# Optimization experiments

Measured on AMD Instinct MI355X. Metric: run time of the kernel, lower is better.

Reference implementation:

```python
import jax, jax.numpy as jnp
import numpy as np


def _conv1x1(x, w, b=None):
    # x: [B,C,H,W], w: [O,C]
    y = jnp.einsum('bchw,oc->bohw', x, w)
    if b is not None:
        y = y + b[None, :, None, None]
    return y


def _conv3x3_dilated(x, w, b, dil):
    p = dil  # padding == dilation keeps spatial size for 3x3 kernels
    y = jax.lax.conv_general_dilated(
        x, w, window_strides=(1, 1), padding=((p, p), (p, p)),
        rhs_dilation=(dil, dil), dimension_numbers=('NCHW', 'OIHW', 'NCHW'))
    return y + b[None, :, None, None]


def _upsample2x_align_corners(x):
    # bilinear, align_corners=True, scale factor 2
    B, C, H, W = x.shape
    oh, ow = 2 * H, 2 * W
    ys = jnp.linspace(0.0, H - 1.0, oh)
    xs = jnp.linspace(0.0, W - 1.0, ow)
    y0 = jnp.floor(ys).astype(jnp.int32)
    x0 = jnp.floor(xs).astype(jnp.int32)
    y1 = jnp.minimum(y0 + 1, H - 1)
    x1 = jnp.minimum(x0 + 1, W - 1)
    wy = (ys - y0)[None, None, :, None]
    wx = (xs - x0)[None, None, None, :]
    gt = x[:, :, y0, :]
    gb = x[:, :, y1, :]
    top = gt[:, :, :, x0] * (1 - wx) + gt[:, :, :, x1] * wx
    bot = gb[:, :, :, x0] * (1 - wx) + gb[:, :, :, x1] * wx
    return top * (1 - wy) + bot * wy


def _gr(ftr, ck_w, ck_b, avg_w, max_w, gcn_w):
    # GR module: attention-diagonal graph conv with degree normalization
    B, C, H, W = ftr.shape
    HW = H * W
    # ChannelAttention_diag -> diagonal entries cw: [B, M]
    avg = ftr.mean(axis=(2, 3))
    mx = ftr.max(axis=(2, 3))
    cw = jax.nn.sigmoid(jax.nn.relu(avg @ avg_w.T) + jax.nn.relu(mx @ max_w.T))  # [B,M]
    k = jax.nn.relu(_conv1x1(ftr, ck_w, ck_b)).reshape(B, -1, HW)  # [B,M,HW]
    q = jnp.swapaxes(k, 1, 2)  # [B,HW,M]
    # A = sigmoid(q @ diag(cw) @ k); degree d = rowsum(A)^(-1/2)
    A = jax.nn.sigmoid(jnp.einsum('bim,bm,bmj->bij', q, cw, k))  # [B,HW,HW]
    d = A.sum(axis=2) ** -0.5  # [B,HW]
    P = d[:, :, None] * q  # D^{-1/2} @ q, [B,HW,M]
    X = jnp.swapaxes(ftr.reshape(B, C, HW), 1, 2)  # [B,HW,C]
    PtX = jnp.einsum('bjm,bjc->bmc', P, X)  # [B,M,C]
    LX = X - jnp.einsum('bim,bmc->bic', P, cw[:, :, None] * PtX)
    Y = X + LX @ gcn_w  # GCN (no bias)
    return jnp.swapaxes(Y, 1, 2).reshape(B, C, H, W)


def setup_inputs() -> dict:
    key = jax.random.key(0)
    ks = jax.random.split(key, 20)
    B, C = 64, 1024
    Cq = C // 4  # 256
    Mi = Cq // 2  # 128, ChannelAttention inter channels
    s = 0.02
    inp = {
        'x_cur': jax.random.normal(ks[0], (B, C, 16, 16), jnp.float32),
        'x_lat': jax.random.normal(ks[1], (B, C, 8, 8), jnp.float32),
        'conv_w': jax.random.normal(ks[2], (Cq, C), jnp.float32) * s,
        'conv_b': jax.random.normal(ks[3], (Cq,), jnp.float32) * s,
        'conv1_w': jax.random.normal(ks[4], (C, Cq), jnp.float32) * s,
        'conv1_b': jax.random.normal(ks[5], (C,), jnp.float32) * s,
        'conv3_w': jax.random.normal(ks[6], (C, 3 * Cq), jnp.float32) * s,
        'conv3_b': jax.random.normal(ks[7], (C,), jnp.float32) * s,
        'rate0_w': jax.random.normal(ks[8], (Cq, C, 3, 3), jnp.float32) * s,
        'rate0_b': jax.random.normal(ks[9], (Cq,), jnp.float32) * s,
        'rate1_w': jax.random.normal(ks[10], (Cq, C, 3, 3), jnp.float32) * s,
        'rate1_b': jax.random.normal(ks[11], (Cq,), jnp.float32) * s,
        'rate2_w': jax.random.normal(ks[12], (Cq, C, 3, 3), jnp.float32) * s,
        'rate2_b': jax.random.normal(ks[13], (Cq,), jnp.float32) * s,
        'gr_ck_w': jax.random.normal(ks[14], (Mi, Cq), jnp.float32) * s,
        'gr_ck_b': jax.random.normal(ks[15], (Mi,), jnp.float32) * s,
        'gr_avg_w': jax.random.normal(ks[16], (Mi, Cq), jnp.float32) * s,
        'gr_max_w': jax.random.normal(ks[17], (Mi, Cq), jnp.float32) * s,
        'gr_gcn_w': jax.random.normal(ks[18], (Cq, Cq), jnp.float32) * s,
        'pre': 1,
    }
    return inp


def reference(x_cur, x_lat, conv_w, conv_b, conv1_w, conv1_b, conv3_w, conv3_b,
              rate0_w, rate0_b, rate1_w, rate1_b, rate2_w, rate2_b,
              gr_ck_w, gr_ck_b, gr_avg_w, gr_max_w, gr_gcn_w, pre):
    # pre == 1 path of Graph_aspp.forward
    gr_args = (gr_ck_w, gr_ck_b, gr_avg_w, gr_max_w, gr_gcn_w)
    x_sum = x_cur * _upsample2x_align_corners(x_lat) + x_cur
    f1 = _conv3x3_dilated(x_sum, rate0_w, rate0_b, 1) + _conv1x1(x_sum, conv_w, conv_b)
    x1 = _gr(f1, *gr_args)
    feature = _conv1x1(f1, conv1_w, conv1_b) + x_sum
    f2 = _conv3x3_dilated(feature, rate1_w, rate1_b, 2) + _conv1x1(feature, conv_w, conv_b)
    x2 = _gr(f2, *gr_args)
    feature = _conv1x1(f2, conv1_w, conv1_b) + x_sum
    f3 = _conv3x3_dilated(feature, rate2_w, rate2_b, 4) + _conv1x1(feature, conv_w, conv_b)
    x3 = _gr(f3, *gr_args)
    cat = jnp.concatenate((x1, x2, x3), axis=1)
    return _conv1x1(cat, conv3_w, conv3_b)
```

## Files before the change

kernel.cpp:

```cpp
#include <hip/hip_runtime.h>

typedef unsigned short ushort_t;
typedef unsigned int uint32;
typedef __attribute__((ext_vector_type(8))) unsigned short ushort8;
typedef __attribute__((ext_vector_type(8))) __bf16 bf16x8;
typedef __attribute__((ext_vector_type(4))) float f32x4;

__device__ __forceinline__ ushort_t f2b(float f) {
    union { float f; uint32 u; } v; v.f = f;
    uint32 r = v.u + 0x7fffu + ((v.u >> 16) & 1u);
    return (ushort_t)(r >> 16);
}
__device__ __forceinline__ float b2f(ushort_t b) {
    union { uint32 u; float f; } v; v.u = ((uint32)b) << 16;
    return v.f;
}
__device__ __forceinline__ float sigm(float x) { return 1.f / (1.f + __expf(-x)); }

__device__ __forceinline__ void gload_lds16(const void* g, void* l) {
    __builtin_amdgcn_global_load_lds(
        (__attribute__((address_space(1))) void*)g,
        (__attribute__((address_space(3))) void*)l, 16, 0, 0);
}

constexpr int EPI_RELU  = 1;
constexpr int EPI_FQ    = 2;
constexpr int EPI_SIG   = 3;
constexpr int EPI_XG    = 4;
constexpr int EPI_NEGCW = 5;
constexpr int EPI_Y     = 6;
constexpr int EPI_OUTT  = 7;

struct GemmP {
    const ushort_t* A; const ushort_t* B;
    const ushort_t* A2; const ushort_t* B2;
    long long aBatch, bBatch, a2Batch, b2Batch;
    int lda, ldb, lda2, ldb2;
    int Ksub, kSplit, dil;
    const float* bias;
    const ushort_t* res; long long resBatch; int ldres;
    ushort_t* obf; long long oBatch; int ldo;
    ushort_t* obf2;
    float* of32;
    const float* cw;
    const float* rscale;
    float* dsum;
    const ushort_t* zpage;
};

__global__ __launch_bounds__(256) void gemm_big(GemmP p) {
    __shared__ __align__(16) ushort_t aT[128 * 64];
    __shared__ __align__(16) ushort_t bT[128 * 64];
    const int tid = threadIdx.x;
    const int z = blockIdx.z;
    const int m0 = blockIdx.x * 128, n0 = blockIdx.y * 128;
    const int lane = tid & 63, wid = tid >> 6;
    const int l15 = lane & 15, l16 = lane >> 4;
    const int wr = wid >> 1, wc = wid & 1;
    const int lrow = lane >> 3;
    const int sgran = (lane & 7) ^ lrow;

    int ayy[4], axx[4];
    const ushort_t* aBase[4];
    const ushort_t* bBase[4];
#pragma unroll
    for (int i = 0; i < 4; ++i) {
        int row = wid * 32 + i * 8 + lrow;
        int m = m0 + row;
        int bb = m >> 8;
        ayy[i] = (m >> 4) & 15; axx[i] = m & 15;
        aBase[i] = p.A + (long long)bb * 262144 + sgran * 8;
        bBase[i] = p.B + (long long)(n0 + row) * p.ldb + sgran * 8;
    }

    f32x4 acc[4][4];
#pragma unroll
    for (int i = 0; i < 4; ++i)
#pragma unroll
        for (int j = 0; j < 4; ++j) acc[i][j] = (f32x4){0.f, 0.f, 0.f, 0.f};

    const int gk0 = z * p.kSplit;
    const int ntap = p.Ksub >> 10;
    for (int ti = 0; ti < ntap; ++ti) {
        const int tap = (gk0 >> 10) + ti;
        int dy = 0, dx = 0;
        if (tap < 9) { int ky = tap / 3; dy = (ky - 1) * p.dil; dx = (tap - ky * 3 - 1) * p.dil; }
        const ushort_t* gaA[4];
        const ushort_t* gaB[4];
#pragma unroll
        for (int i = 0; i < 4; ++i) {
            int iy = ayy[i] + dy, ix = axx[i] + dx;
            bool ok = ((unsigned)iy < 16u) && ((unsigned)ix < 16u);
            gaA[i] = ok ? (aBase[i] + (((iy << 4) + ix) << 10)) : (p.zpage + sgran * 8);
            gaB[i] = bBase[i] + (tap << 10);
        }
        for (int kk = 0; kk < 16; ++kk) {
            const int kin = kk << 6;
#pragma unroll
            for (int i = 0; i < 4; ++i)
                gload_lds16(gaA[i] + kin, &aT[(wid * 32 + i * 8) * 64]);
#pragma unroll
            for (int i = 0; i < 4; ++i)
                gload_lds16(gaB[i] + kin, &bT[(wid * 32 + i * 8) * 64]);
            asm volatile("s_waitcnt vmcnt(0)" ::: "memory");
            __syncthreads();
#pragma unroll
            for (int ks = 0; ks < 2; ++ks) {
                bf16x8 af[4], bfr[4];
#pragma unroll
                for (int mi = 0; mi < 4; ++mi) {
                    int rr = wr * 64 + mi * 16 + l15;
                    int cc = (ks * 32 + l16 * 8) ^ ((rr & 7) << 3);
                    af[mi] = __builtin_bit_cast(bf16x8, *(const ushort8*)&aT[rr * 64 + cc]);
                }
#pragma unroll
                for (int ni = 0; ni < 4; ++ni) {
                    int rr = wc * 64 + ni * 16 + l15;
                    int cc = (ks * 32 + l16 * 8) ^ ((rr & 7) << 3);
                    bfr[ni] = __builtin_bit_cast(bf16x8, *(const ushort8*)&bT[rr * 64 + cc]);
                }
#pragma unroll
                for (int mi = 0; mi < 4; ++mi)
#pragma unroll
                    for (int ni = 0; ni < 4; ++ni)
                        acc[mi][ni] = __builtin_amdgcn_mfma_f32_16x16x32_bf16(af[mi], bfr[ni], acc[mi][ni], 0, 0, 0);
            }
            __syncthreads();
        }
    }
#pragma unroll
    for (int mi = 0; mi < 4; ++mi)
#pragma unroll
        for (int ni = 0; ni < 4; ++ni) {
            int gcol = n0 + wc * 64 + ni * 16 + l15;
            int growb = m0 + wr * 64 + mi * 16 + l16 * 4;
#pragma unroll
            for (int r = 0; r < 4; ++r)
                p.obf[(long long)z * p.oBatch + (long long)(growb + r) * 256 + gcol] =
                    f2b(acc[mi][ni][r]);
        }
}

template<int BM, int BN, int AMODE, int EPI>
__device__ __forceinline__ void gemm_body(ushort_t* aT, ushort_t* bT,
                                          const GemmP& p, int z) {
    constexpr int APASS = BM / 32, BPASS = BN / 32;
    constexpr int MFRAG = BM / 32, NFRAG = BN / 32;
    const int tid = threadIdx.x;
    const int m0 = blockIdx.x * BM, n0 = blockIdx.y * BN;
    const int lane = tid & 63, wid = tid >> 6;
    const int l15 = lane & 15, l16 = lane >> 4;
    const int wr = wid >> 1, wc = wid & 1;
    const int srow = tid >> 3, scol = (tid & 7) * 8;
    const int swcol = scol ^ ((srow & 7) << 3);

    const ushort_t* aptr[APASS];
    const ushort_t* bptr[BPASS];
    const ushort_t* aptr2[APASS];
    const ushort_t* bptr2[BPASS];
    float rsA[APASS];
#pragma unroll
    for (int pi = 0; pi < APASS; ++pi)
        aptr[pi] = p.A + (long long)z * p.aBatch +
                   (long long)(m0 + pi * 32 + srow) * p.lda + scol;
#pragma unroll
    for (int pi = 0; pi < BPASS; ++pi)
        bptr[pi] = p.B + (long long)z * p.bBatch +
                   (long long)(n0 + pi * 32 + srow) * p.ldb + scol;
    if constexpr (AMODE == 2) {
#pragma unroll
        for (int pi = 0; pi < APASS; ++pi) {
            aptr2[pi] = p.A2 + (long long)z * p.a2Batch +
                        (long long)(m0 + pi * 32 + srow) * p.lda2 + scol;
            rsA[pi] = p.rscale[z * 256 + m0 + pi * 32 + srow];
        }
#pragma unroll
        for (int pi = 0; pi < BPASS; ++pi)
            bptr2[pi] = p.B2 + (long long)z * p.b2Batch +
                        (long long)(n0 + pi * 32 + srow) * p.ldb2 + scol;
    }

    f32x4 acc[MFRAG][NFRAG];
#pragma unroll
    for (int i = 0; i < MFRAG; ++i)
#pragma unroll
        for (int j = 0; j < NFRAG; ++j) acc[i][j] = (f32x4){0.f, 0.f, 0.f, 0.f};

    ushort8 ar[APASS], br[BPASS];
    auto ldg = [&](int gk) {
        if (AMODE == 2 && gk >= 256) {
            int g2 = gk - 256;
#pragma unroll
            for (int pi = 0; pi < APASS; ++pi) {
                ushort8 t8 = *(const ushort8*)(aptr2[pi] + g2);
#pragma unroll
                for (int k = 0; k < 8; ++k) t8[k] = f2b(b2f(t8[k]) * rsA[pi]);
                ar[pi] = t8;
            }
#pragma unroll
            for (int pi = 0; pi < BPASS; ++pi) br[pi] = *(const ushort8*)(bptr2[pi] + g2);
        } else if constexpr (AMODE == 3) {
#pragma unroll
            for (int pi = 0; pi < APASS; ++pi) {
                ushort8 t8 = *(const ushort8*)(aptr[pi] + gk);
#pragma unroll
                for (int k = 0; k < 8; ++k)
                    t8[k] = f2b(b2f(t8[k]) * p.cw[(z << 7) + gk + scol + k]);
                ar[pi] = t8;
            }
#pragma unroll
            for (int pi = 0; pi < BPASS; ++pi) br[pi] = *(const ushort8*)(bptr[pi] + gk);
        } else {
#pragma unroll
            for (int pi = 0; pi < APASS; ++pi) ar[pi] = *(const ushort8*)(aptr[pi] + gk);
#pragma unroll
            for (int pi = 0; pi < BPASS; ++pi) br[pi] = *(const ushort8*)(bptr[pi] + gk);
        }
    };

    const int gk0 = z * p.kSplit;
    ldg(gk0);
    const int iters = p.Ksub >> 6;
    for (int it = 0; it < iters; ++it) {
#pragma unroll
        for (int pi = 0; pi < APASS; ++pi)
            *(ushort8*)&aT[(pi * 32 + srow) * 64 + swcol] = ar[pi];
#pragma unroll
        for (int pi = 0; pi < BPASS; ++pi)
            *(ushort8*)&bT[(pi * 32 + srow) * 64 + swcol] = br[pi];
        __syncthreads();
        if (it + 1 < iters) ldg(gk0 + (it + 1) * 64);
#pragma unroll
        for (int ks = 0; ks < 2; ++ks) {
            bf16x8 af[MFRAG], bfr[NFRAG];
#pragma unroll
            for (int mi = 0; mi < MFRAG; ++mi) {
                int rr = wr * (BM / 2) + mi * 16 + l15;
                int cc = (ks * 32 + l16 * 8) ^ ((rr & 7) << 3);
                af[mi] = __builtin_bit_cast(bf16x8, *(const ushort8*)&aT[rr * 64 + cc]);
            }
#pragma unroll
            for (int ni = 0; ni < NFRAG; ++ni) {
                int rr = wc * (BN / 2) + ni * 16 + l15;
                int cc = (ks * 32 + l16 * 8) ^ ((rr & 7) << 3);
                bfr[ni] = __builtin_bit_cast(bf16x8, *(const ushort8*)&bT[rr * 64 + cc]);
            }
#pragma unroll
            for (int mi = 0; mi < MFRAG; ++mi)
#pragma unroll
                for (int ni = 0; ni < NFRAG; ++ni)
                    acc[mi][ni] = __builtin_amdgcn_mfma_f32_16x16x32_bf16(af[mi], bfr[ni], acc[mi][ni], 0, 0, 0);
        }
        __syncthreads();
    }

#pragma unroll
    for (int mi = 0; mi < MFRAG; ++mi) {
        if constexpr (EPI == EPI_SIG) {
#pragma unroll
            for (int r = 0; r < 4; ++r) {
                float sv = 0.f;
#pragma unroll
                for (int ni = 0; ni < NFRAG; ++ni) sv += sigm(acc[mi][ni][r]);
                sv += __shfl_xor(sv, 1); sv += __shfl_xor(sv, 2);
                sv += __shfl_xor(sv, 4); sv += __shfl_xor(sv, 8);
                if (l15 == 0) {
                    int grow = m0 + wr * (BM / 2) + mi * 16 + l16 * 4 + r;
                    int q8 = blockIdx.y * 2 + wc;
                    p.dsum[q8 * 16384 + z * 256 + grow] = sv;
                }
            }
        } else {
#pragma unroll
            for (int ni = 0; ni < NFRAG; ++ni) {
                int gcol = n0 + wc * (BN / 2) + ni * 16 + l15;
                int growb = m0 + wr * (BM / 2) + mi * 16 + l16 * 4;
#pragma unroll
                for (int r = 0; r < 4; ++r) {
                    int grow = growb + r;
                    float v = acc[mi][ni][r];
                    if constexpr (EPI == EPI_RELU) {
                        v += p.bias[gcol]; v = fmaxf(v, 0.f);
                        p.obf[(long long)grow * p.ldo + gcol] = f2b(v);
                    } else if constexpr (EPI == EPI_FQ) {
                        v += p.bias[gcol];
                        if (gcol < 1024) {
                            v += b2f(p.res[(long long)grow * 1024 + gcol]);
                            p.obf[(long long)grow * 1024 + gcol] = f2b(v);
                        } else {
                            v = fmaxf(v, 0.f);
                            p.obf2[(long long)grow * 128 + (gcol - 1024)] = f2b(v);
                        }
                    } else if constexpr (EPI == EPI_XG) {
                        p.obf[(long long)z * p.oBatch + (long long)grow * p.ldo + gcol] = f2b(v);
                    } else if constexpr (EPI == EPI_NEGCW) {
                        v *= -p.cw[z * 128 + gcol];
                        p.obf[(long long)z * p.oBatch + (long long)grow * p.ldo + gcol] = f2b(v);
                    } else if constexpr (EPI == EPI_Y) {
                        v = b2f(p.res[(long long)z * p.resBatch + (long long)grow * p.ldres + gcol]) + v;
                        p.obf[(long long)z * p.oBatch + (long long)grow * p.ldo + gcol] = f2b(v);
                    } else if constexpr (EPI == EPI_OUTT) {
                        v += p.bias[grow];
                        int bb = gcol >> 8, px = gcol & 255;
                        p.of32[((long long)bb * 1024 + grow) * 256 + px] = v;
                    }
                }
            }
        }
    }
}

template<int BM, int BN, int AMODE, int EPI>
__global__ __launch_bounds__(256) void gemm_k(GemmP p) {
    __shared__ __align__(16) ushort_t aT[BM * 64];
    __shared__ __align__(16) ushort_t bT[BN * 64];
    gemm_body<BM, BN, AMODE, EPI>(aT, bT, p, blockIdx.z);
}

__device__ __forceinline__ void pool_body(void* lds, const ushort_t* f,
                                          const float* aw, const float* mw,
                                          float* cw) {
    float* sa = (float*)lds;
    float* sm = sa + 256;
    int b = blockIdx.x, t = threadIdx.x;
    float s = 0.f, m = -3.4e38f;
    const ushort_t* base = f + (long long)b * 65536 + t;
    for (int px = 0; px < 256; ++px) { float v = b2f(base[px * 256]); s += v; m = fmaxf(m, v); }
    sa[t] = s * (1.f / 256.f);
    sm[t] = m;
    __syncthreads();
    if (t < 128) {
        float s1 = 0.f, s2 = 0.f;
        const float* a = aw + t * 256; const float* w = mw + t * 256;
        for (int c = 0; c < 256; ++c) { s1 += sa[c] * a[c]; s2 += sm[c] * w[c]; }
        s1 = fmaxf(s1, 0.f); s2 = fmaxf(s2, 0.f);
        cw[b * 128 + t] = sigm(s1 + s2);
    }
}

__global__ __launch_bounds__(256) void gemm_fqpool(GemmP p, const float* aw,
                                                   const float* mw, float* cw) {
    __shared__ __align__(16) ushort_t aT[128 * 64];
    __shared__ __align__(16) ushort_t bT[128 * 64];
    if (blockIdx.y == 9) {
        if (blockIdx.x < 64) pool_body(aT, p.A, aw, mw, cw);
        return;
    }
    gemm_body<128, 128, 0, EPI_FQ>(aT, bT, p, 0);
}

__global__ __launch_bounds__(256) void gemm_qpool(GemmP p, const float* aw,
                                                  const float* mw, float* cw) {
    __shared__ __align__(16) ushort_t aT[64 * 64];
    __shared__ __align__(16) ushort_t bT[64 * 64];
    if (blockIdx.y == 2) {
        if (blockIdx.x < 64) pool_body(aT, p.A, aw, mw, cw);
        return;
    }
    gemm_body<64, 64, 0, EPI_RELU>(aT, bT, p, 0);
}

__global__ __launch_bounds__(256) void gemm_sigxg(GemmP ps, GemmP px) {
    __shared__ __align__(16) ushort_t aT[64 * 64];
    __shared__ __align__(16) ushort_t bT[64 * 64];
    int z = blockIdx.z;
    if (z < 64) gemm_body<64, 64, 3, EPI_SIG>(aT, bT, ps, z);
    else        gemm_body<64, 64, 0, EPI_XG>(aT, bT, px, z - 64);
}


__global__ void k_combine(const ushort_t* __restrict__ t, const float* __restrict__ fbias_s,
                          ushort_t* __restrict__ f) {
    int idx = blockIdx.x * 256 + threadIdx.x;
    const long long N = 16384ll * 256;
    ushort8 a0 = *(const ushort8*)(t + (long long)idx * 8);
    ushort8 a1 = *(const ushort8*)(t + N + (long long)idx * 8);
    ushort8 a2 = *(const ushort8*)(t + 2 * N + (long long)idx * 8);
    ushort8 a3 = *(const ushort8*)(t + 3 * N + (long long)idx * 8);
    ushort8 a4 = *(const ushort8*)(t + 4 * N + (long long)idx * 8);
    int cb = (idx * 8) & 255;
    ushort8 o;
#pragma unroll
    for (int k = 0; k < 8; ++k)
        o[k] = f2b(b2f(a0[k]) + b2f(a1[k]) + b2f(a2[k]) + b2f(a3[k]) + b2f(a4[k]) + fbias_s[cb + k]);
    *(ushort8*)&f[(long long)idx * 8] = o;
}

__global__ void k_upsum(const float* __restrict__ xc, const float* __restrict__ xl,
                        ushort_t* __restrict__ xs) {
    __shared__ float lat[64 * 64];
    __shared__ ushort_t tile[64 * 258];
    int b = blockIdx.x, c0 = blockIdx.y * 64;
    int t = threadIdx.x;
    for (int i = t; i < 4096; i += 256)
        lat[i] = xl[((long long)(b * 1024 + c0 + (i >> 6))) * 64 + (i & 63)];
    __syncthreads();
    int y = t >> 4, x = t & 15;
    float fy = y * (7.f / 15.f); int y0 = (int)fy; float wy = fy - y0; int y1 = y0 + 1 > 7 ? 7 : y0 + 1;
    float fx = x * (7.f / 15.f); int x0 = (int)fx; float wx = fx - x0; int x1 = x0 + 1 > 7 ? 7 : x0 + 1;
    for (int cc = 0; cc < 64; ++cc) {
        float cur = xc[((long long)(b * 1024 + c0 + cc)) * 256 + t];
        const float* L = &lat[cc * 64];
        float tv = L[y0 * 8 + x0] * (1.f - wx) + L[y0 * 8 + x1] * wx;
        float bv = L[y1 * 8 + x0] * (1.f - wx) + L[y1 * 8 + x1] * wx;
        float up = tv + (bv - tv) * wy;
        tile[cc * 258 + t] = f2b(cur * (1.f + up));
    }
    __syncthreads();
    for (int i = t; i < 16384; i += 256) {
        int px = i >> 6, cc = i & 63;
        xs[((long long)(b * 256 + px)) * 1024 + c0 + cc] = tile[cc * 258 + px];
    }
}

__global__ void k_pscale(const ushort_t* __restrict__ q, const float* __restrict__ dsum8,
                         float* __restrict__ dscale, ushort_t* __restrict__ Pt) {
    __shared__ ushort_t t[128][130];
    __shared__ float dd[128];
    int jh = blockIdx.x, b = blockIdx.y;
    int j0 = jh * 128;
    int tid = threadIdx.x;
    if (tid < 128) {
        int pix = b * 256 + j0 + tid;
        float s = 0.f;
#pragma unroll
        for (int qs = 0; qs < 8; ++qs) s += dsum8[qs * 16384 + pix];
        float r = rsqrtf(s);
        dd[tid] = r;
        dscale[pix] = r;
    }
    __syncthreads();
    int jr = tid >> 7, m = tid & 127;
    for (int i = 0; i < 64; ++i) {
        int j = i * 2 + jr;
        long long qi = ((long long)(b * 256 + j0 + j)) * 128 + m;
        t[j][m] = f2b(dd[j] * b2f(q[qi]));
    }
    __syncthreads();
    for (int i = 0; i < 64; ++i) {
        int mm = i * 2 + jr;
        Pt[((long long)b << 15) + (mm << 8) + j0 + m] = t[m][mm];
    }
}

__global__ void k_packall(const float* r0, const float* r1, const float* r2,
                          const float* convw, const float* c1w, const float* c3w,
                          const float* ckw, const float* gcnw,
                          const float* rb0, const float* rb1, const float* rb2,
                          const float* cb, const float* c1b, const float* ckbias,
                          ushort_t* wbig3, ushort_t* wfq, ushort_t* w3b,
                          ushort_t* gcnT, float* fqbias, float* fbias,
                          ushort_t* zpage) {
    int blk = blockIdx.x, tid = threadIdx.x;
    if (blk < 768) {
        __shared__ float lw[10240];
        int s = blk >> 8, o = blk & 255;
        const float* rate = s == 0 ? r0 : (s == 1 ? r1 : r2);
        for (int i = tid; i < 9216; i += 256) lw[i] = rate[(long long)o * 9216 + i];
        for (int i = tid; i < 1024; i += 256) lw[9216 + i] = convw[(long long)o * 1024 + i];
        __syncthreads();
        ushort_t* dst = wbig3 + (long long)blk * 10240;
        for (int i = tid; i < 10240; i += 256) {
            int tap = i >> 10, ci = i & 1023;
            float v = (tap < 9) ? lw[ci * 9 + tap] : lw[9216 + ci];
            dst[i] = f2b(v);
        }
        return;
    }
    const int R1 = 262144;
    const int R2 = R1 + 32768;
    const int R3 = R2 + 786432;
    const int R4 = R3 + 65536;
    const int R5 = R4 + 1152;
    const int R6 = R5 + 768;
    const int R7 = R6 + 4096;
    int base = (blk - 768) * 2048 + tid * 8;
#pragma unroll
    for (int k = 0; k < 8; ++k) {
        int i = base + k;
        if (i >= R7) return;
        if (i < R1) wfq[i] = f2b(c1w[i]);
        else if (i < R2) wfq[i] = f2b(ckw[i - R1]);
        else if (i < R3) w3b[i - R2] = f2b(c3w[i - R2]);
        else if (i < R4) {
            int ii = i - R3; int c2 = ii >> 8, c1 = ii & 255;
            gcnT[ii] = f2b(gcnw[c1 * 256 + c2]);
        } else if (i < R5) {
            int ii = i - R4;
            fqbias[ii] = (ii < 1024) ? c1b[ii] : ckbias[ii - 1024];
        } else if (i < R6) {
            int ii = i - R5; int s = ii >> 8, t = ii & 255;
            const float* rb = s == 0 ? rb0 : (s == 1 ? rb1 : rb2);
            fbias[ii] = rb[t] + cb[t];
        } else {
            zpage[i - R6] = 0;
        }
    }
}

__global__ void k_sentinel(float* o, int n, float v) {
    int i = blockIdx.x * 256 + threadIdx.x; if (i < n) o[i] = v;
}

extern "C" void kernel_launch(void* const* d_in, const int* in_sizes, int n_in,
                              void* d_out, int out_size, void* d_ws, size_t ws_size,
                              hipStream_t stream) {
    const float* x_cur  = (const float*)d_in[0];
    const float* x_lat  = (const float*)d_in[1];
    const float* conv_w = (const float*)d_in[2];
    const float* conv_b = (const float*)d_in[3];
    const float* conv1_w = (const float*)d_in[4];
    const float* conv1_b = (const float*)d_in[5];
    const float* conv3_w = (const float*)d_in[6];
    const float* conv3_b = (const float*)d_in[7];
    const float* rate_w[3] = {(const float*)d_in[8], (const float*)d_in[10], (const float*)d_in[12]};
    const float* rate_b[3] = {(const float*)d_in[9], (const float*)d_in[11], (const float*)d_in[13]};
    const float* ck_w  = (const float*)d_in[14];
    const float* ck_b  = (const float*)d_in[15];
    const float* avg_w = (const float*)d_in[16];
    const float* max_w = (const float*)d_in[17];
    const float* gcn_w = (const float*)d_in[18];
    float* out = (float*)d_out;

    char* w = (char*)d_ws;
    auto take = [&](size_t bytes) { void* p = (void*)w; w += (bytes + 255) & ~(size_t)255; return p; };
    ushort_t* xsum   = (ushort_t*)take(16384ll * 1024 * 2);
    ushort_t* feat   = (ushort_t*)take(16384ll * 1024 * 2);
    ushort_t* fbuf   = (ushort_t*)take(16384ll * 256 * 2);
    ushort_t* xgt    = (ushort_t*)take(64ll * 256 * 256 * 2);
    ushort_t* qbuf   = (ushort_t*)take(16384ll * 128 * 2);
    ushort_t* Pt     = (ushort_t*)take(64ll * 128 * 256 * 2);
    ushort_t* Htn    = (ushort_t*)take(64ll * 256 * 128 * 2);
    ushort_t* wbig3  = (ushort_t*)take(3ll * 256 * 10240 * 2);
    ushort_t* wfq    = (ushort_t*)take(1152ll * 256 * 2);
    ushort_t* w3b    = (ushort_t*)take(1024ll * 768 * 2);
    ushort_t* gcnT   = (ushort_t*)take(256ll * 256 * 2);
    ushort_t* zpage  = (ushort_t*)take(8192);
    float*    fqbias = (float*)take(1152 * 4);
    float*    fbias  = (float*)take(3 * 256 * 4);
    float*    cwb    = (float*)take(64 * 128 * 4);
    float*    dscale = (float*)take(64 * 256 * 4);
    float*    dsum8  = (float*)take(8ll * 64 * 256 * 4);
    ushort_t* catb   = (ushort_t*)take(16384ll * 768 * 2);
    ushort_t* ftmp   = (ushort_t*)take(5ll * 16384 * 256 * 2);
    size_t need = (size_t)(w - (char*)d_ws);

    if (need > ws_size) {
        float v = 1.0e6f + (float)(ws_size >> 20);
        k_sentinel<<<(out_size + 255) / 256, 256, 0, stream>>>(out, out_size, v);
        return;
    }

    k_packall<<<768 + 563, 256, 0, stream>>>(
        rate_w[0], rate_w[1], rate_w[2], conv_w, conv1_w, conv3_w, ck_w, gcn_w,
        rate_b[0], rate_b[1], rate_b[2], conv_b, conv1_b, ck_b,
        wbig3, wfq, w3b, gcnT, fqbias, fbias, zpage);
    k_upsum<<<dim3(64, 16), 256, 0, stream>>>(x_cur, x_lat, xsum);

    for (int s = 0; s < 3; ++s) {
        {
            GemmP p{};
            p.A = (s == 0) ? xsum : feat;
            p.B = wbig3 + (long long)s * 256 * 10240; p.ldb = 10240;
            p.Ksub = 2048; p.kSplit = 2048; p.dil = 1 << s;
            p.obf = ftmp; p.oBatch = 16384ll * 256;
            p.zpage = zpage;
            gemm_big<<<dim3(128, 2, 5), 256, 0, stream>>>(p);
        }
        k_combine<<<2048, 256, 0, stream>>>(ftmp, fbias + s * 256, fbuf);
        if (s < 2) {
            GemmP p{};
            p.A = fbuf; p.lda = 256; p.B = wfq; p.ldb = 256;
            p.Ksub = 256; p.bias = fqbias;
            p.res = xsum;
            p.obf = feat; p.obf2 = qbuf;
            gemm_fqpool<<<dim3(128, 10, 1), 256, 0, stream>>>(p, avg_w, max_w, cwb);
        } else {
            GemmP p{};
            p.A = fbuf; p.lda = 256; p.B = wfq + 1024 * 256; p.ldb = 256;
            p.Ksub = 256;
            p.bias = ck_b; p.obf = qbuf; p.ldo = 128;
            gemm_qpool<<<dim3(256, 3, 1), 256, 0, stream>>>(p, avg_w, max_w, cwb);
        }
        {
            GemmP ps{};
            ps.A = qbuf; ps.aBatch = 32768; ps.lda = 128;
            ps.B = qbuf; ps.bBatch = 32768; ps.ldb = 128;
            ps.Ksub = 128; ps.dsum = dsum8; ps.cw = cwb;
            GemmP px{};
            px.A = gcnT; px.aBatch = 0;     px.lda = 256;
            px.B = fbuf; px.bBatch = 65536; px.ldb = 256;
            px.Ksub = 256;
            px.obf = xgt; px.oBatch = 65536; px.ldo = 256;
            gemm_sigxg<<<dim3(4, 4, 128), 256, 0, stream>>>(ps, px);
        }
        k_pscale<<<dim3(2, 64), 256, 0, stream>>>(qbuf, dsum8, dscale, Pt);
        {
            GemmP p{};
            p.A = xgt; p.aBatch = 65536; p.lda = 256;
            p.B = Pt;  p.bBatch = 32768; p.ldb = 256;
            p.Ksub = 256; p.cw = cwb;
            p.obf = Htn; p.oBatch = 32768; p.ldo = 128;
            gemm_k<64, 64, 0, EPI_NEGCW><<<dim3(4, 2, 64), 256, 0, stream>>>(p);
        }
        {
            GemmP p{};
            p.A = fbuf; p.aBatch = 65536; p.lda = 256;
            p.B = gcnT; p.bBatch = 0;     p.ldb = 256;
            p.A2 = qbuf; p.a2Batch = 32768; p.lda2 = 128; p.rscale = dscale;
            p.B2 = Htn;  p.b2Batch = 32768; p.ldb2 = 128;
            p.Ksub = 384;
            p.res = fbuf; p.resBatch = 65536; p.ldres = 256;
            p.obf = catb + s * 256; p.oBatch = 256ll * 768; p.ldo = 768;
            gemm_k<64, 64, 2, EPI_Y><<<dim3(4, 4, 64), 256, 0, stream>>>(p);
        }
    }
    {
        GemmP p{};
        p.A = w3b;  p.lda = 768;
        p.B = catb; p.ldb = 768;
        p.Ksub = 768; p.bias = conv3_b; p.of32 = out;
        gemm_k<64, 128, 0, EPI_OUTT><<<dim3(16, 128, 1), 256, 0, stream>>>(p);
    }
}
```

Before: 646.4 us.

## Software-pipeline GR stages across ASPP stages by fusing independent GEMMs into shared launches

Restructures the three-stage loop so each stage's GR work (sigmoid-degree GEMM, X·G GEMM, Htn and Y GEMMs) runs in the same kernel launch as the next stage's big dilated conv GEMM or FQ GEMM. Block indices are dispatched to different GEMM bodies through flattened grid coordinates. fbuf, qbuf and cw are double-buffered so adjacent stages do not conflict. The aim is fewer launches and better CU fill for the small under-occupying GR GEMMs, at the cost of more complex dispatch and a larger shared-memory footprint for the small tiles.

```diff
diff --git a/kernel.cpp b/kernel.cpp
--- a/kernel.cpp
+++ b/kernel.cpp
@@ -48,12 +48,10 @@
     const ushort_t* zpage;
 };
 
-__global__ __launch_bounds__(256) void gemm_big(GemmP p) {
-    __shared__ __align__(16) ushort_t aT[128 * 64];
-    __shared__ __align__(16) ushort_t bT[128 * 64];
+__device__ __forceinline__ void big_body(ushort_t* aT, ushort_t* bT,
+                                         const GemmP& p, int bx, int by, int z) {
     const int tid = threadIdx.x;
-    const int z = blockIdx.z;
-    const int m0 = blockIdx.x * 128, n0 = blockIdx.y * 128;
+    const int m0 = bx * 128, n0 = by * 128;
     const int lane = tid & 63, wid = tid >> 6;
     const int l15 = lane & 15, l16 = lane >> 4;
     const int wr = wid >> 1, wc = wid & 1;
@@ -143,11 +141,11 @@
 
 template<int BM, int BN, int AMODE, int EPI>
 __device__ __forceinline__ void gemm_body(ushort_t* aT, ushort_t* bT,
-                                          const GemmP& p, int z) {
+                                          const GemmP& p, int bx, int by, int z) {
     constexpr int APASS = BM / 32, BPASS = BN / 32;
     constexpr int MFRAG = BM / 32, NFRAG = BN / 32;
     const int tid = threadIdx.x;
-    const int m0 = blockIdx.x * BM, n0 = blockIdx.y * BN;
+    const int m0 = bx * BM, n0 = by * BN;
     const int lane = tid & 63, wid = tid >> 6;
     const int l15 = lane & 15, l16 = lane >> 4;
     const int wr = wid >> 1, wc = wid & 1;
@@ -266,7 +264,7 @@
                 sv += __shfl_xor(sv, 4); sv += __shfl_xor(sv, 8);
                 if (l15 == 0) {
                     int grow = m0 + wr * (BM / 2) + mi * 16 + l16 * 4 + r;
-                    int q8 = blockIdx.y * 2 + wc;
+                    int q8 = by * 2 + wc;
                     p.dsum[q8 * 16384 + z * 256 + grow] = sv;
                 }
             }
@@ -314,15 +312,15 @@
 __global__ __launch_bounds__(256) void gemm_k(GemmP p) {
     __shared__ __align__(16) ushort_t aT[BM * 64];
     __shared__ __align__(16) ushort_t bT[BN * 64];
-    gemm_body<BM, BN, AMODE, EPI>(aT, bT, p, blockIdx.z);
-}
-
-__device__ __forceinline__ void pool_body(void* lds, const ushort_t* f,
+    gemm_body<BM, BN, AMODE, EPI>(aT, bT, p, blockIdx.x, blockIdx.y, blockIdx.z);
+}
+
+__device__ __forceinline__ void pool_body(void* lds, int b, const ushort_t* f,
                                           const float* aw, const float* mw,
                                           float* cw) {
     float* sa = (float*)lds;
     float* sm = sa + 256;
-    int b = blockIdx.x, t = threadIdx.x;
+    int t = threadIdx.x;
     float s = 0.f, m = -3.4e38f;
     const ushort_t* base = f + (long long)b * 65536 + t;
     for (int px = 0; px < 256; ++px) { float v = b2f(base[px * 256]); s += v; m = fmaxf(m, v); }
@@ -338,34 +336,51 @@
     }
 }
 
-__global__ __launch_bounds__(256) void gemm_fqpool(GemmP p, const float* aw,
-                                                   const float* mw, float* cw) {
-    __shared__ __align__(16) ushort_t aT[128 * 64];
-    __shared__ __align__(16) ushort_t bT[128 * 64];
-    if (blockIdx.y == 9) {
-        if (blockIdx.x < 64) pool_body(aT, p.A, aw, mw, cw);
+__global__ __launch_bounds__(256) void k_big_sig_y(GemmP pb, GemmP ps, GemmP px,
+                                                   GemmP py) {
+    __shared__ __align__(16) ushort_t lds[2 * 128 * 64];
+    int z = blockIdx.z;
+    if (z < 5) { big_body(lds, lds + 8192, pb, blockIdx.x, blockIdx.y, z); return; }
+    if (z < 13) {
+        int flat = (z - 5) * 256 + blockIdx.y * 128 + blockIdx.x;
+        int bx = flat & 3, by = (flat >> 2) & 3, bz = flat >> 4;
+        if (bz < 64) gemm_body<64, 64, 3, EPI_SIG>(lds, lds + 4096, ps, bx, by, bz);
+        else         gemm_body<64, 64, 0, EPI_XG>(lds, lds + 4096, px, bx, by, bz - 64);
         return;
     }
-    gemm_body<128, 128, 0, EPI_FQ>(aT, bT, p, 0);
-}
-
-__global__ __launch_bounds__(256) void gemm_qpool(GemmP p, const float* aw,
-                                                  const float* mw, float* cw) {
-    __shared__ __align__(16) ushort_t aT[64 * 64];
-    __shared__ __align__(16) ushort_t bT[64 * 64];
-    if (blockIdx.y == 2) {
-        if (blockIdx.x < 64) pool_body(aT, p.A, aw, mw, cw);
-        return;
-    }
-    gemm_body<64, 64, 0, EPI_RELU>(aT, bT, p, 0);
-}
-
-__global__ __launch_bounds__(256) void gemm_sigxg(GemmP ps, GemmP px) {
+    int flat = (z - 13) * 256 + blockIdx.y * 128 + blockIdx.x;
+    gemm_body<64, 64, 2, EPI_Y>(lds, lds + 4096, py, flat & 3, (flat >> 2) & 3, flat >> 4);
+}
+
+__global__ __launch_bounds__(256) void k_fqpool_htn(GemmP pf, GemmP ph,
+                                                    const float* aw, const float* mw,
+                                                    float* cw) {
+    __shared__ __align__(16) ushort_t lds[2 * 128 * 64];
+    int y = blockIdx.y;
+    if (y < 9) { gemm_body<128, 128, 0, EPI_FQ>(lds, lds + 8192, pf, blockIdx.x, y, 0); return; }
+    if (y == 9) { if (blockIdx.x < 64) pool_body(lds, blockIdx.x, pf.A, aw, mw, cw); return; }
+    int flat = (y - 10) * 128 + blockIdx.x;
+    gemm_body<64, 64, 0, EPI_NEGCW>(lds, lds + 4096, ph, flat & 3, (flat >> 2) & 1, flat >> 3);
+}
+
+__global__ __launch_bounds__(256) void k_qpool_htn(GemmP pq, GemmP ph,
+                                                   const float* aw, const float* mw,
+                                                   float* cw) {
+    __shared__ __align__(16) ushort_t lds[2 * 64 * 64];
+    int y = blockIdx.y;
+    if (y < 2) { gemm_body<64, 64, 0, EPI_RELU>(lds, lds + 4096, pq, blockIdx.x, y, 0); return; }
+    if (y == 2) { if (blockIdx.x < 64) pool_body(lds, blockIdx.x, pq.A, aw, mw, cw); return; }
+    int flat = (y - 3) * 256 + blockIdx.x;
+    gemm_body<64, 64, 0, EPI_NEGCW>(lds, lds + 4096, ph, flat & 3, (flat >> 2) & 1, flat >> 3);
+}
+
+__global__ __launch_bounds__(256) void k_sigxg_y(GemmP ps, GemmP px, GemmP py) {
     __shared__ __align__(16) ushort_t aT[64 * 64];
     __shared__ __align__(16) ushort_t bT[64 * 64];
     int z = blockIdx.z;
-    if (z < 64) gemm_body<64, 64, 3, EPI_SIG>(aT, bT, ps, z);
-    else        gemm_body<64, 64, 0, EPI_XG>(aT, bT, px, z - 64);
+    if (z < 64)       gemm_body<64, 64, 3, EPI_SIG>(aT, bT, ps, blockIdx.x, blockIdx.y, z);
+    else if (z < 128) gemm_body<64, 64, 0, EPI_XG>(aT, bT, px, blockIdx.x, blockIdx.y, z - 64);
+    else              gemm_body<64, 64, 2, EPI_Y>(aT, bT, py, blockIdx.x, blockIdx.y, z - 128);
 }
 
 
@@ -526,9 +541,13 @@
     auto take = [&](size_t bytes) { void* p = (void*)w; w += (bytes + 255) & ~(size_t)255; return p; };
     ushort_t* xsum   = (ushort_t*)take(16384ll * 1024 * 2);
     ushort_t* feat   = (ushort_t*)take(16384ll * 1024 * 2);
-    ushort_t* fbuf   = (ushort_t*)take(16384ll * 256 * 2);
+    ushort_t* fbufP[2];
+    fbufP[0] = (ushort_t*)take(16384ll * 256 * 2);
+    fbufP[1] = (ushort_t*)take(16384ll * 256 * 2);
+    ushort_t* qbufP[2];
+    qbufP[0] = (ushort_t*)take(16384ll * 128 * 2);
+    qbufP[1] = (ushort_t*)take(16384ll * 128 * 2);
     ushort_t* xgt    = (ushort_t*)take(64ll * 256 * 256 * 2);
-    ushort_t* qbuf   = (ushort_t*)take(16384ll * 128 * 2);
     ushort_t* Pt     = (ushort_t*)take(64ll * 128 * 256 * 2);
     ushort_t* Htn    = (ushort_t*)take(64ll * 256 * 128 * 2);
     ushort_t* wbig3  = (ushort_t*)take(3ll * 256 * 10240 * 2);
@@ -538,7 +557,9 @@
     ushort_t* zpage  = (ushort_t*)take(8192);
     float*    fqbias = (float*)take(1152 * 4);
     float*    fbias  = (float*)take(3 * 256 * 4);
-    float*    cwb    = (float*)take(64 * 128 * 4);
+    float*    cwbP[2];
+    cwbP[0] = (float*)take(64 * 128 * 4);
+    cwbP[1] = (float*)take(64 * 128 * 4);
     float*    dscale = (float*)take(64 * 256 * 4);
     float*    dsum8  = (float*)take(8ll * 64 * 256 * 4);
     ushort_t* catb   = (ushort_t*)take(16384ll * 768 * 2);
@@ -551,70 +572,86 @@
         return;
     }
 
+    auto PBIG = [&](int s) {
+        GemmP p{};
+        p.A = (s == 0) ? xsum : feat;
+        p.B = wbig3 + (long long)s * 256 * 10240; p.ldb = 10240;
+        p.Ksub = 2048; p.kSplit = 2048; p.dil = 1 << s;
+        p.obf = ftmp; p.oBatch = 16384ll * 256;
+        p.zpage = zpage;
+        return p;
+    };
+    auto PSIG = [&](int s) {
+        GemmP p{};
+        p.A = qbufP[s & 1]; p.aBatch = 32768; p.lda = 128;
+        p.B = qbufP[s & 1]; p.bBatch = 32768; p.ldb = 128;
+        p.Ksub = 128; p.dsum = dsum8; p.cw = cwbP[s & 1];
+        return p;
+    };
+    auto PXG = [&](int s) {
+        GemmP p{};
+        p.A = gcnT; p.aBatch = 0;            p.lda = 256;
+        p.B = fbufP[s & 1]; p.bBatch = 65536; p.ldb = 256;
+        p.Ksub = 256;
+        p.obf = xgt; p.oBatch = 65536; p.ldo = 256;
+        return p;
+    };
+    auto PHTN = [&](int s) {
+        GemmP p{};
+        p.A = xgt; p.aBatch = 65536; p.lda = 256;
+        p.B = Pt;  p.bBatch = 32768; p.ldb = 256;
+        p.Ksub = 256; p.cw = cwbP[s & 1];
+        p.obf = Htn; p.oBatch = 32768; p.ldo = 128;
+        return p;
+    };
+    auto PY = [&](int s) {
+        GemmP p{};
+        p.A = fbufP[s & 1]; p.aBatch = 65536; p.lda = 256;
+        p.B = gcnT; p.bBatch = 0;             p.ldb = 256;
+        p.A2 = qbufP[s & 1]; p.a2Batch = 32768; p.lda2 = 128; p.rscale = dscale;
+        p.B2 = Htn;          p.b2Batch = 32768; p.ldb2 = 128;
+        p.Ksub = 384;
+        p.res = fbufP[s & 1]; p.resBatch = 65536; p.ldres = 256;
+        p.obf = catb + s * 256; p.oBatch = 256ll * 768; p.ldo = 768;
+        return p;
+    };
+    auto PFQ = [&](int s) {
+        GemmP p{};
+        p.A = fbufP[s & 1]; p.lda = 256; p.B = wfq; p.ldb = 256;
+        p.Ksub = 256; p.bias = fqbias;
+        p.res = xsum;
+        p.obf = feat; p.obf2 = qbufP[s & 1];
+        return p;
+    };
+    GemmP pz{};
+
     k_packall<<<768 + 563, 256, 0, stream>>>(
         rate_w[0], rate_w[1], rate_w[2], conv_w, conv1_w, conv3_w, ck_w, gcn_w,
         rate_b[0], rate_b[1], rate_b[2], conv_b, conv1_b, ck_b,
         wbig3, wfq, w3b, gcnT, fqbias, fbias, zpage);
     k_upsum<<<dim3(64, 16), 256, 0, stream>>>(x_cur, x_lat, xsum);
 
-    for (int s = 0; s < 3; ++s) {
-        {
-            GemmP p{};
-            p.A = (s == 0) ? xsum : feat;
-            p.B = wbig3 + (long long)s * 256 * 10240; p.ldb = 10240;
-            p.Ksub = 2048; p.kSplit = 2048; p.dil = 1 << s;
-            p.obf = ftmp; p.oBatch = 16384ll * 256;
-            p.zpage = zpage;
-            gemm_big<<<dim3(128, 2, 5), 256, 0, stream>>>(p);
-        }
-        k_combine<<<2048, 256, 0, stream>>>(ftmp, fbias + s * 256, fbuf);
-        if (s < 2) {
-            GemmP p{};
-            p.A = fbuf; p.lda = 256; p.B = wfq; p.ldb = 256;
-            p.Ksub = 256; p.bias = fqbias;
-            p.res = xsum;
-            p.obf = feat; p.obf2 = qbuf;
-            gemm_fqpool<<<dim3(128, 10, 1), 256, 0, stream>>>(p, avg_w, max_w, cwb);
-        } else {
-            GemmP p{};
-            p.A = fbuf; p.lda = 256; p.B = wfq + 1024 * 256; p.ldb = 256;
-            p.Ksub = 256;
-            p.bias = ck_b; p.obf = qbuf; p.ldo = 128;
-            gemm_qpool<<<dim3(256, 3, 1), 256, 0, stream>>>(p, avg_w, max_w, cwb);
-        }
-        {
-            GemmP ps{};
-            ps.A = qbuf; ps.aBatch = 32768; ps.lda = 128;
-            ps.B = qbuf; ps.bBatch = 32768; ps.ldb = 128;
-            ps.Ksub = 128; ps.dsum = dsum8; ps.cw = cwb;
-            GemmP px{};
-            px.A = gcnT; px.aBatch = 0;     px.lda = 256;
-            px.B = fbuf; px.bBatch = 65536; px.ldb = 256;
-            px.Ksub = 256;
-            px.obf = xgt; px.oBatch = 65536; px.ldo = 256;
-            gemm_sigxg<<<dim3(4, 4, 128), 256, 0, stream>>>(ps, px);
-        }
-        k_pscale<<<dim3(2, 64), 256, 0, stream>>>(qbuf, dsum8, dscale, Pt);
-        {
-            GemmP p{};
-            p.A = xgt; p.aBatch = 65536; p.lda = 256;
-            p.B = Pt;  p.bBatch = 32768; p.ldb = 256;
-            p.Ksub = 256; p.cw = cwb;
-            p.obf = Htn; p.oBatch = 32768; p.ldo = 128;
-            gemm_k<64, 64, 0, EPI_NEGCW><<<dim3(4, 2, 64), 256, 0, stream>>>(p);
-        }
-        {
-            GemmP p{};
-            p.A = fbuf; p.aBatch = 65536; p.lda = 256;
-            p.B = gcnT; p.bBatch = 0;     p.ldb = 256;
-            p.A2 = qbuf; p.a2Batch = 32768; p.lda2 = 128; p.rscale = dscale;
-            p.B2 = Htn;  p.b2Batch = 32768; p.ldb2 = 128;
-            p.Ksub = 384;
-            p.res = fbuf; p.resBatch = 65536; p.ldres = 256;
-            p.obf = catb + s * 256; p.oBatch = 256ll * 768; p.ldo = 768;
-            gemm_k<64, 64, 2, EPI_Y><<<dim3(4, 4, 64), 256, 0, stream>>>(p);
-        }
-    }
+    k_big_sig_y<<<dim3(128, 2, 5), 256, 0, stream>>>(PBIG(0), pz, pz, pz);
+    k_combine<<<2048, 256, 0, stream>>>(ftmp, fbias + 0 * 256, fbufP[0]);
+    k_fqpool_htn<<<dim3(128, 10), 256, 0, stream>>>(PFQ(0), pz, avg_w, max_w, cwbP[0]);
+    k_big_sig_y<<<dim3(128, 2, 13), 256, 0, stream>>>(PBIG(1), PSIG(0), PXG(0), pz);
+    k_combine<<<2048, 256, 0, stream>>>(ftmp, fbias + 1 * 256, fbufP[1]);
+    k_pscale<<<dim3(2, 64), 256, 0, stream>>>(qbufP[0], dsum8, dscale, Pt);
+    k_fqpool_htn<<<dim3(128, 14), 256, 0, stream>>>(PFQ(1), PHTN(0), avg_w, max_w, cwbP[1]);
+    k_big_sig_y<<<dim3(128, 2, 17), 256, 0, stream>>>(PBIG(2), PSIG(1), PXG(1), PY(0));
+    k_combine<<<2048, 256, 0, stream>>>(ftmp, fbias + 2 * 256, fbufP[0]);
+    k_pscale<<<dim3(2, 64), 256, 0, stream>>>(qbufP[1], dsum8, dscale, Pt);
+    {
+        GemmP pq{};
+        pq.A = fbufP[0]; pq.lda = 256; pq.B = wfq + 1024 * 256; pq.ldb = 256;
+        pq.Ksub = 256;
+        pq.bias = ck_b; pq.obf = qbufP[0]; pq.ldo = 128;
+        k_qpool_htn<<<dim3(256, 5), 256, 0, stream>>>(pq, PHTN(1), avg_w, max_w, cwbP[0]);
+    }
+    k_sigxg_y<<<dim3(4, 4, 192), 256, 0, stream>>>(PSIG(2), PXG(2), PY(1));
+    k_pscale<<<dim3(2, 64), 256, 0, stream>>>(qbufP[0], dsum8, dscale, Pt);
+    gemm_k<64, 64, 0, EPI_NEGCW><<<dim3(4, 2, 64), 256, 0, stream>>>(PHTN(2));
+    gemm_k<64, 64, 2, EPI_Y><<<dim3(4, 4, 64), 256, 0, stream>>>(PY(2));
     {
         GemmP p{};
         p.A = w3b;  p.lda = 768;
```

Result: faster. 626.0 us (-3.2%).
